# Optimization experiments

Measured on AMD Instinct MI355X. Metric: run time of the kernel, lower is better.

Reference implementation:

```python
import jax, jax.numpy as jnp
import numpy as np

D_MODEL = 1024
NUM_HEADS = 16
DK = D_MODEL // NUM_HEADS


def setup_inputs() -> dict:
    key = jax.random.key(0)
    ks = jax.random.split(key, 12)
    B, S, D = 2, 2048, D_MODEL
    s = 1.0 / np.sqrt(D)
    inp = {
        "Q": jax.random.normal(ks[0], (B, S, D), jnp.float32),
        "K": jax.random.normal(ks[1], (B, S, D), jnp.float32),
        "V": jax.random.normal(ks[2], (B, S, D), jnp.float32),
        "Wq": jax.random.uniform(ks[3], (D, D), jnp.float32, -s, s),
        "bq": jax.random.uniform(ks[4], (D,), jnp.float32, -s, s),
        "Wk": jax.random.uniform(ks[5], (D, D), jnp.float32, -s, s),
        "bk": jax.random.uniform(ks[6], (D,), jnp.float32, -s, s),
        "Wv": jax.random.uniform(ks[7], (D, D), jnp.float32, -s, s),
        "bv": jax.random.uniform(ks[8], (D,), jnp.float32, -s, s),
        "Wo": jax.random.uniform(ks[9], (D, D), jnp.float32, -s, s),
        "bo": jax.random.uniform(ks[10], (D,), jnp.float32, -s, s),
    }
    return inp


def reference(Q, K, V, Wq, bq, Wk, bk, Wv, bv, Wo, bo):
    B, S, D = Q.shape
    H, dk = NUM_HEADS, DK
    # projections (torch Linear: x @ W.T + b), split heads -> [B,H,S,dk]
    q = (Q @ Wq.T + bq).reshape(B, S, H, dk).transpose(0, 2, 1, 3)
    k = (K @ Wk.T + bk).reshape(B, S, H, dk).transpose(0, 2, 1, 3)
    v = (V @ Wv.T + bv).reshape(B, S, H, dk).transpose(0, 2, 1, 3)
    scores = jnp.einsum("bhqd,bhkd->bhqk", q, k) / jnp.sqrt(jnp.asarray(dk, q.dtype))
    attn = jax.nn.softmax(scores, axis=-1)
    out = jnp.einsum("bhqk,bhkd->bhqd", attn, v)  # [B,H,S,dk]
    out = out.transpose(0, 2, 1, 3).reshape(B, S, D)
    return out @ Wo.T + bo
```

## Files before the change

### kernel.cpp

```cpp
#include <hip/hip_runtime.h>
#include <stdint.h>


#define AS1 __attribute__((address_space(1)))
#define AS3 __attribute__((address_space(3)))

typedef unsigned short u16;
typedef short s16x8 __attribute__((ext_vector_type(8)));
typedef float f32x4 __attribute__((ext_vector_type(4)));
typedef float f32x16 __attribute__((ext_vector_type(16)));
typedef u16   u16x4 __attribute__((ext_vector_type(4)));

#if defined(__has_builtin)
#if __has_builtin(__builtin_amdgcn_exp2f)
#define EXP2F(x) __builtin_amdgcn_exp2f(x)
#else
#define EXP2F(x) exp2f(x)
#endif
#else
#define EXP2F(x) exp2f(x)
#endif

__device__ __forceinline__ u16 f2b(float f) {
  union { float f; uint32_t u; } v;
  v.f = f;
  uint32_t r = (v.u + 0x7fffu + ((v.u >> 16) & 1u)) >> 16;
  return (u16)r;
}

__device__ __forceinline__ uint32_t cvtpk(float lo, float hi) {
  uint32_t r;
  asm("v_cvt_pk_bf16_f32 %0, %1, %2" : "=v"(r) : "v"(lo), "v"(hi));
  return r;
}

__device__ __forceinline__ float max3f(float a, float b, float c) {
  float r;
  asm("v_max3_f32 %0, %1, %2, %3" : "=v"(r) : "v"(a), "v"(b), "v"(c));
  return r;
}

__device__ __forceinline__ f32x4 mfma16(s16x8 a, s16x8 b, f32x4 c) {
  return __builtin_amdgcn_mfma_f32_16x16x32_bf16(a, b, c, 0, 0, 0);
}

__device__ __forceinline__ f32x16 mfma32(s16x8 a, s16x8 b, f32x16 c) {
  return __builtin_amdgcn_mfma_f32_32x32x16_bf16(a, b, c, 0, 0, 0);
}

__device__ __forceinline__ s16x8 ld_g16(const u16* p) {
  return *reinterpret_cast<const s16x8*>(p);
}

__device__ __forceinline__ void stage16(const u16* g, u16* lds_base) {
  __builtin_amdgcn_global_load_lds((const AS1 unsigned int*)g,
                                   (AS3 unsigned int*)lds_base, 16, 0, 0);
}

struct CvtArgs {
  const float* src[4];
  u16* dst[4];
  int cum[5];
};

__global__ __launch_bounds__(256) void cvt_all(CvtArgs a) {
  const int bx = blockIdx.x;
  int seg = 0;
#pragma unroll
  for (int i = 1; i < 4; ++i) seg += (bx >= a.cum[i]) ? 1 : 0;
  const int off = (bx - a.cum[seg]) * 256 + threadIdx.x;
  float4 f = reinterpret_cast<const float4*>(a.src[seg])[off];
  union { u16 u[4]; uint64_t q; } o;
  o.u[0] = f2b(f.x); o.u[1] = f2b(f.y); o.u[2] = f2b(f.z); o.u[3] = f2b(f.w);
  reinterpret_cast<uint64_t*>(a.dst[seg])[off] = o.q;
}

template <int MODE>
__global__ __launch_bounds__(256) void gemm_bt(const float* __restrict__ Aq,
                                               const float* __restrict__ Ak,
                                               const float* __restrict__ Av,
                                               const u16* __restrict__ Abf,
                                               const u16* __restrict__ Wbase,
                                               const float* __restrict__ bias0,
                                               const float* __restrict__ bias1,
                                               const float* __restrict__ bias2,
                                               u16* __restrict__ outb,
                                               u16* __restrict__ vtout,
                                               float* __restrict__ outf) {
  __shared__ u16 As[2][128 * 64];
  __shared__ u16 Bs[2][128 * 64];
  const int tid = threadIdx.x;
  const int lane = tid & 63;
  const int w = tid >> 6;
  const int wr = w >> 1, wc = w & 1;

  const int bid = blockIdx.y * 8 + blockIdx.x;
  const int sw = (bid & 7) * 32 + (bid >> 3);
  const int n0 = (sw & 7) * 128;
  const int m0 = (sw >> 3) * 128;
  const int z = (MODE == 0) ? blockIdx.z : 0;
  const float QSC = 0.18033688011112042f;

  const float* Af = (MODE == 0) ? (z == 0 ? Aq : (z == 1 ? Ak : Av)) : nullptr;
  const u16* W = Wbase + (size_t)z * (1024u * 1024u);
  const float* bias = (MODE == 0) ? (z == 0 ? bias0 : (z == 1 ? bias1 : bias2)) : bias0;
  u16* ob = (MODE == 0) ? (outb + (size_t)z * (4096u * 1024u)) : nullptr;

  const int l15 = lane & 15, l4 = lane >> 4;

  const int sr = lane >> 3;
  const int sx = lane & 7;
  const float* gAf[4];
  const u16* gAb[4];
  const u16* gB[4];
#pragma unroll
  for (int j = 0; j < 4; ++j) {
    const int row = w * 32 + j * 8 + sr;
    const int lc = ((sx ^ (row & 7)) << 3);
    if (MODE == 0) gAf[j] = Af + (size_t)(m0 + row) * 1024 + lc;
    else           gAb[j] = Abf + (size_t)(m0 + row) * 1024 + lc;
    gB[j] = W + (size_t)(n0 + row) * 1024 + lc;
  }

  f32x4 acc[4][4];
#pragma unroll
  for (int i = 0; i < 4; ++i)
#pragma unroll
    for (int j = 0; j < 4; ++j) acc[i][j] = {0.f, 0.f, 0.f, 0.f};

#pragma unroll
  for (int j = 0; j < 4; ++j) {
    if (MODE == 0) {
      float4 b0 = *(const float4*)gAf[j];
      float4 b1 = *(const float4*)(gAf[j] + 4);
      union { uint32_t d[4]; s16x8 v; } cv;
      cv.d[0] = cvtpk(b0.x, b0.y); cv.d[1] = cvtpk(b0.z, b0.w);
      cv.d[2] = cvtpk(b1.x, b1.y); cv.d[3] = cvtpk(b1.z, b1.w);
      *(s16x8*)&As[0][(w * 32 + j * 8) * 64 + lane * 8] = cv.v;
    } else {
      stage16(gAb[j], &As[0][(w * 32 + j * 8) * 64]);
    }
    stage16(gB[j], &Bs[0][(w * 32 + j * 8) * 64]);
  }
  __syncthreads();

#pragma unroll 2
  for (int t = 0; t < 16; ++t) {
    const int cur = t & 1;
    float4 a0[4], a1[4];
    const bool more = (t + 1 < 16);
    if (more) {
      const int kt = (t + 1) * 64;
      if (MODE == 0) {
#pragma unroll
        for (int j = 0; j < 4; ++j) {
          a0[j] = *(const float4*)(gAf[j] + kt);
          a1[j] = *(const float4*)(gAf[j] + kt + 4);
        }
      } else {
#pragma unroll
        for (int j = 0; j < 4; ++j)
          stage16(gAb[j] + kt, &As[cur ^ 1][(w * 32 + j * 8) * 64]);
      }
#pragma unroll
      for (int j = 0; j < 4; ++j)
        stage16(gB[j] + kt, &Bs[cur ^ 1][(w * 32 + j * 8) * 64]);
    }
#pragma unroll
    for (int ks = 0; ks < 2; ++ks) {
      s16x8 af[4], bf[4];
#pragma unroll
      for (int mi = 0; mi < 4; ++mi) {
        const int row = wr * 64 + mi * 16 + l15;
        const int sc_ = (((ks << 2) | l4) ^ (l15 & 7)) << 3;
        af[mi] = *(const s16x8*)&As[cur][row * 64 + sc_];
      }
#pragma unroll
      for (int ni = 0; ni < 4; ++ni) {
        const int row = wc * 64 + ni * 16 + l15;
        const int sc_ = (((ks << 2) | l4) ^ (l15 & 7)) << 3;
        bf[ni] = *(const s16x8*)&Bs[cur][row * 64 + sc_];
      }
      __builtin_amdgcn_s_setprio(1);
#pragma unroll
      for (int mi = 0; mi < 4; ++mi)
#pragma unroll
        for (int ni = 0; ni < 4; ++ni)
          acc[mi][ni] = mfma16(af[mi], bf[ni], acc[mi][ni]);
      __builtin_amdgcn_s_setprio(0);
    }
    if (more && MODE == 0) {
#pragma unroll
      for (int j = 0; j < 4; ++j) {
        union { uint32_t d[4]; s16x8 v; } cv;
        cv.d[0] = cvtpk(a0[j].x, a0[j].y); cv.d[1] = cvtpk(a0[j].z, a0[j].w);
        cv.d[2] = cvtpk(a1[j].x, a1[j].y); cv.d[3] = cvtpk(a1[j].z, a1[j].w);
        *(s16x8*)&As[cur ^ 1][(w * 32 + j * 8) * 64 + lane * 8] = cv.v;
      }
    }
    __syncthreads();
  }

#pragma unroll
  for (int ni = 0; ni < 4; ++ni) {
    const int col = n0 + wc * 64 + ni * 16 + l15;
    const float bv = bias[col];
#pragma unroll
    for (int mi = 0; mi < 4; ++mi) {
      const int row0 = m0 + wr * 64 + mi * 16 + l4 * 4;
      if (MODE == 0 && z == 2) {
        const int b = row0 >> 11, s0 = row0 & 2047;
        const int pos0 = (s0 & ~15) | ((s0 & 4) << 1) | ((s0 & 8) >> 1);
        const int h = col >> 6, d = col & 63;
        u16x4 pk = {f2b(acc[mi][ni][0] + bv), f2b(acc[mi][ni][1] + bv),
                    f2b(acc[mi][ni][2] + bv), f2b(acc[mi][ni][3] + bv)};
        *(u16x4*)&vtout[((size_t)(b * 16 + h) * 64 + d) * 2048 + pos0] = pk;
      } else {
#pragma unroll
        for (int r = 0; r < 4; ++r) {
          float val = acc[mi][ni][r] + bv;
          const int row = row0 + r;
          if (MODE == 0) {
            if (z == 0) val *= QSC;
            const int b = row >> 11, s = row & 2047;
            const int h = col >> 6, d = col & 63;
            ob[((size_t)(b * 16 + h) * 2048 + s) * 64 + d] = f2b(val);
          } else {
            outf[(size_t)row * 1024 + col] = val;
          }
        }
      }
    }
  }
}

__global__ __launch_bounds__(512, 2) void fattn(const u16* __restrict__ qp,
                                                const u16* __restrict__ kp,
                                                const u16* __restrict__ vt,
                                                u16* __restrict__ ao) {
  __shared__ u16 Kt[2][4096];
  __shared__ u16 Vt[2][4096];

  const int lane = threadIdx.x & 63;
  const int w = threadIdx.x >> 6;
  const int bh = blockIdx.y;
  const int b = bh >> 4, h = bh & 15;
  const int q0 = blockIdx.x * 256 + w * 32;
  const u16* qb = qp + (size_t)bh * (2048 * 64);
  const u16* kb = kp + (size_t)bh * (2048 * 64);
  const u16* vb = vt + (size_t)bh * (64 * 2048);
  const int l31 = lane & 31, hl = lane >> 5;
  const int x7 = l31 & 7;
  const float THR = 8.0f;

  const int srow = (w << 3) + (lane >> 3);
  const int c0 = (((lane & 7) ^ (srow & 7)) << 3);

  s16x8 qa[4];
#pragma unroll
  for (int kc = 0; kc < 4; ++kc)
    qa[kc] = ld_g16(qb + (size_t)(q0 + l31) * 64 + kc * 16 + hl * 8);

  f32x16 o[2];
  float lsum = 0.f;
  float mrun = 0.f;
#pragma unroll
  for (int r = 0; r < 16; ++r) { o[0][r] = 0.f; o[1][r] = 0.f; }

  stage16(kb + (size_t)srow * 64 + c0, &Kt[0][w * 512]);
  stage16(vb + (size_t)srow * 2048 + c0, &Vt[0][w * 512]);
  __syncthreads();

#pragma unroll 2
  for (int t = 0; t < 32; ++t) {
    const int cur = t & 1;
    if (t + 1 < 32) {
      const int kk = (t + 1) << 6;
      stage16(kb + (size_t)(kk + srow) * 64 + c0, &Kt[cur ^ 1][w * 512]);
      stage16(vb + (size_t)srow * 2048 + kk + c0, &Vt[cur ^ 1][w * 512]);
    }

    f32x16 sc[2];
#pragma unroll
    for (int r = 0; r < 16; ++r) { sc[0][r] = -mrun; sc[1][r] = -mrun; }
#pragma unroll
    for (int nk = 0; nk < 2; ++nk) {
      s16x8 kf[4];
#pragma unroll
      for (int kc = 0; kc < 4; ++kc)
        kf[kc] = *(const s16x8*)&Kt[cur][(nk * 32 + l31) * 64 +
                                         ((((kc << 1) | hl) ^ x7) << 3)];
      __builtin_amdgcn_s_setprio(1);
#pragma unroll
      for (int kc = 0; kc < 4; ++kc)
        sc[nk] = mfma32(kf[kc], qa[kc], sc[nk]);
      __builtin_amdgcn_s_setprio(0);
    }

    float m = -1e30f;
#pragma unroll
    for (int nk = 0; nk < 2; ++nk)
#pragma unroll
      for (int r = 0; r < 16; r += 2)
        m = max3f(m, sc[nk][r], sc[nk][r + 1]);
    m = fmaxf(m, __shfl_xor(m, 32));

    if (__any(m > THR)) {
      const float d = fmaxf(m, 0.f);
      mrun += d;
      const float alpha = EXP2F(-d);
      lsum *= alpha;
#pragma unroll
      for (int r = 0; r < 16; ++r) { sc[0][r] -= d; sc[1][r] -= d; }
#pragma unroll
      for (int r = 0; r < 16; ++r) {
        float ar = __shfl(alpha, (r & 3) + 8 * (r >> 2) + 4 * hl);
        o[0][r] *= ar; o[1][r] *= ar;
      }
    }

#pragma unroll
    for (int nk = 0; nk < 2; ++nk) {
      float p[16];
#pragma unroll
      for (int r = 0; r < 16; ++r) p[r] = EXP2F(sc[nk][r]);
#pragma unroll
      for (int r = 0; r < 16; ++r) lsum += p[r];
#pragma unroll
      for (int kc = 0; kc < 2; ++kc) {
        union { uint32_t d[4]; s16x8 v; } pa;
        pa.d[0] = cvtpk(p[kc * 8 + 0], p[kc * 8 + 1]);
        pa.d[1] = cvtpk(p[kc * 8 + 2], p[kc * 8 + 3]);
        pa.d[2] = cvtpk(p[kc * 8 + 4], p[kc * 8 + 5]);
        pa.d[3] = cvtpk(p[kc * 8 + 6], p[kc * 8 + 7]);
        const int chunk = nk * 4 + kc * 2 + hl;
#pragma unroll
        for (int dt = 0; dt < 2; ++dt) {
          s16x8 vf = *(const s16x8*)&Vt[cur][(dt * 32 + l31) * 64 +
                                             ((chunk ^ x7) << 3)];
          __builtin_amdgcn_s_setprio(1);
          o[dt] = mfma32(pa.v, vf, o[dt]);
          __builtin_amdgcn_s_setprio(0);
        }
      }
    }

    __syncthreads();
  }

  lsum += __shfl_xor(lsum, 32);
#pragma unroll
  for (int r = 0; r < 16; ++r) {
    const int qreg = (r & 3) + 8 * (r >> 2) + 4 * hl;
    const float inv = 1.0f / __shfl(lsum, qreg);
    const int row = b * 2048 + q0 + qreg;
#pragma unroll
    for (int dt = 0; dt < 2; ++dt)
      ao[(size_t)row * 1024 + h * 64 + dt * 32 + l31] = f2b(o[dt][r] * inv);
  }
}

extern "C" void kernel_launch(void* const* d_in, const int* in_sizes, int n_in,
                              void* d_out, int out_size, void* d_ws, size_t ws_size,
                              hipStream_t stream) {
  const float* Q  = (const float*)d_in[0];
  const float* K  = (const float*)d_in[1];
  const float* V  = (const float*)d_in[2];
  const float* Wq = (const float*)d_in[3];
  const float* bq = (const float*)d_in[4];
  const float* Wk = (const float*)d_in[5];
  const float* bk = (const float*)d_in[6];
  const float* Wv = (const float*)d_in[7];
  const float* bv = (const float*)d_in[8];
  const float* Wo = (const float*)d_in[9];
  const float* bo = (const float*)d_in[10];
  float* out = (float*)d_out;

  const size_t NI = (size_t)4096 * 1024;
  const size_t NW = (size_t)1024 * 1024;
  u16* WB  = (u16*)d_ws;
  u16* QKV = WB + 4 * NW;
  u16* VT  = QKV + 3 * NI;
  u16* AO  = VT + NI;

  CvtArgs ca;
  ca.src[0] = Wq; ca.dst[0] = WB;
  ca.src[1] = Wk; ca.dst[1] = WB + NW;
  ca.src[2] = Wv; ca.dst[2] = WB + 2 * NW;
  ca.src[3] = Wo; ca.dst[3] = WB + 3 * NW;
  ca.cum[0] = 0; ca.cum[1] = 1024; ca.cum[2] = 2048; ca.cum[3] = 3072; ca.cum[4] = 4096;
  cvt_all<<<dim3(4096), 256, 0, stream>>>(ca);

  gemm_bt<0><<<dim3(8, 32, 3), 256, 0, stream>>>(Q, K, V, nullptr, WB, bq, bk, bv,
                                                 QKV, VT, nullptr);
  fattn<<<dim3(8, 32), 512, 0, stream>>>(QKV, QKV + NI, VT, AO);
  gemm_bt<1><<<dim3(8, 32, 1), 256, 0, stream>>>(nullptr, nullptr, nullptr, AO,
                                                 WB + 3 * NW, bo, nullptr, nullptr,
                                                 nullptr, nullptr, out);
}
```

Measured before the change: 121.4 us.

## Triple-buffer LDS and use partial vmcnt barriers in projection GEMM and attention

The attention kernel moves from double- to triple-buffered K/V tiles, staging two tiles ahead. Each iteration now waits with a partial vmcnt on an explicit s_barrier instead of a full __syncthreads, so global loads stay in flight across the barrier. The fp32-input projection GEMM gets a hand-unrolled pipeline: a three-slot A buffer, global loads issued two tiles ahead into alternating register sets, and the bf16 convert/store overlapped with the MFMA work. This adds LDS use (which may cut occupancy for the 512-thread, two-blocks-per-CU attention kernel) and more registers, and it depends on the hand-set vmcnt counts being correct.

```diff
diff --git a/kernel.cpp b/kernel.cpp
--- a/kernel.cpp
+++ b/kernel.cpp
@@ -20,6 +20,14 @@
 #else
 #define EXP2F(x) exp2f(x)
 #endif
+
+#define BARC(N)                                                               \
+  do {                                                                        \
+    __builtin_amdgcn_sched_barrier(0);                                        \
+    asm volatile("s_waitcnt vmcnt(" #N ") lgkmcnt(0)" ::: "memory");          \
+    __builtin_amdgcn_s_barrier();                                             \
+    __builtin_amdgcn_sched_barrier(0);                                        \
+  } while (0)
 
 __device__ __forceinline__ u16 f2b(float f) {
   union { float f; uint32_t u; } v;
@@ -87,8 +95,8 @@
                                                u16* __restrict__ outb,
                                                u16* __restrict__ vtout,
                                                float* __restrict__ outf) {
-  __shared__ u16 As[2][128 * 64];
-  __shared__ u16 Bs[2][128 * 64];
+  __shared__ u16 As[3 * 8192];
+  __shared__ u16 Bs[2][8192];
   const int tid = threadIdx.x;
   const int lane = tid & 63;
   const int w = tid >> 6;
@@ -128,44 +136,11 @@
 #pragma unroll
     for (int j = 0; j < 4; ++j) acc[i][j] = {0.f, 0.f, 0.f, 0.f};
 
-#pragma unroll
-  for (int j = 0; j < 4; ++j) {
-    if (MODE == 0) {
-      float4 b0 = *(const float4*)gAf[j];
-      float4 b1 = *(const float4*)(gAf[j] + 4);
-      union { uint32_t d[4]; s16x8 v; } cv;
-      cv.d[0] = cvtpk(b0.x, b0.y); cv.d[1] = cvtpk(b0.z, b0.w);
-      cv.d[2] = cvtpk(b1.x, b1.y); cv.d[3] = cvtpk(b1.z, b1.w);
-      *(s16x8*)&As[0][(w * 32 + j * 8) * 64 + lane * 8] = cv.v;
-    } else {
-      stage16(gAb[j], &As[0][(w * 32 + j * 8) * 64]);
-    }
-    stage16(gB[j], &Bs[0][(w * 32 + j * 8) * 64]);
-  }
-  __syncthreads();
-
-#pragma unroll 2
-  for (int t = 0; t < 16; ++t) {
-    const int cur = t & 1;
-    float4 a0[4], a1[4];
-    const bool more = (t + 1 < 16);
-    if (more) {
-      const int kt = (t + 1) * 64;
-      if (MODE == 0) {
-#pragma unroll
-        for (int j = 0; j < 4; ++j) {
-          a0[j] = *(const float4*)(gAf[j] + kt);
-          a1[j] = *(const float4*)(gAf[j] + kt + 4);
-        }
-      } else {
-#pragma unroll
-        for (int j = 0; j < 4; ++j)
-          stage16(gAb[j] + kt, &As[cur ^ 1][(w * 32 + j * 8) * 64]);
-      }
-#pragma unroll
-      for (int j = 0; j < 4; ++j)
-        stage16(gB[j] + kt, &Bs[cur ^ 1][(w * 32 + j * 8) * 64]);
-    }
+  auto G_STAGEW = [&](int kt, u16* bbuf) {
+#pragma unroll
+    for (int j = 0; j < 4; ++j) stage16(gB[j] + kt, &bbuf[(w * 32 + j * 8) * 64]);
+  };
+  auto G_MFMA = [&](int aoff, const u16* bbuf) {
 #pragma unroll
     for (int ks = 0; ks < 2; ++ks) {
       s16x8 af[4], bf[4];
@@ -173,13 +148,13 @@
       for (int mi = 0; mi < 4; ++mi) {
         const int row = wr * 64 + mi * 16 + l15;
         const int sc_ = (((ks << 2) | l4) ^ (l15 & 7)) << 3;
-        af[mi] = *(const s16x8*)&As[cur][row * 64 + sc_];
+        af[mi] = *(const s16x8*)&As[aoff + row * 64 + sc_];
       }
 #pragma unroll
       for (int ni = 0; ni < 4; ++ni) {
         const int row = wc * 64 + ni * 16 + l15;
         const int sc_ = (((ks << 2) | l4) ^ (l15 & 7)) << 3;
-        bf[ni] = *(const s16x8*)&Bs[cur][row * 64 + sc_];
+        bf[ni] = *(const s16x8*)&bbuf[row * 64 + sc_];
       }
       __builtin_amdgcn_s_setprio(1);
 #pragma unroll
@@ -189,16 +164,88 @@
           acc[mi][ni] = mfma16(af[mi], bf[ni], acc[mi][ni]);
       __builtin_amdgcn_s_setprio(0);
     }
-    if (more && MODE == 0) {
+  };
+
+  if (MODE == 0) {
+    float4 se0[4], se1[4], so0[4], so1[4];
+    auto G_ISSUE_E = [&](int kt) {
+#pragma unroll
+      for (int j = 0; j < 4; ++j) { se0[j] = *(const float4*)(gAf[j] + kt);
+                                    se1[j] = *(const float4*)(gAf[j] + kt + 4); }
+    };
+    auto G_ISSUE_O = [&](int kt) {
+#pragma unroll
+      for (int j = 0; j < 4; ++j) { so0[j] = *(const float4*)(gAf[j] + kt);
+                                    so1[j] = *(const float4*)(gAf[j] + kt + 4); }
+    };
+    auto G_CVT_E = [&](int aoff) {
 #pragma unroll
       for (int j = 0; j < 4; ++j) {
         union { uint32_t d[4]; s16x8 v; } cv;
-        cv.d[0] = cvtpk(a0[j].x, a0[j].y); cv.d[1] = cvtpk(a0[j].z, a0[j].w);
-        cv.d[2] = cvtpk(a1[j].x, a1[j].y); cv.d[3] = cvtpk(a1[j].z, a1[j].w);
-        *(s16x8*)&As[cur ^ 1][(w * 32 + j * 8) * 64 + lane * 8] = cv.v;
-      }
+        cv.d[0] = cvtpk(se0[j].x, se0[j].y); cv.d[1] = cvtpk(se0[j].z, se0[j].w);
+        cv.d[2] = cvtpk(se1[j].x, se1[j].y); cv.d[3] = cvtpk(se1[j].z, se1[j].w);
+        *(s16x8*)&As[aoff + (w * 32 + j * 8) * 64 + lane * 8] = cv.v;
+      }
+    };
+    auto G_CVT_O = [&](int aoff) {
+#pragma unroll
+      for (int j = 0; j < 4; ++j) {
+        union { uint32_t d[4]; s16x8 v; } cv;
+        cv.d[0] = cvtpk(so0[j].x, so0[j].y); cv.d[1] = cvtpk(so0[j].z, so0[j].w);
+        cv.d[2] = cvtpk(so1[j].x, so1[j].y); cv.d[3] = cvtpk(so1[j].z, so1[j].w);
+        *(s16x8*)&As[aoff + (w * 32 + j * 8) * 64 + lane * 8] = cv.v;
+      }
+    };
+
+    G_STAGEW(0, Bs[0]);
+    G_ISSUE_E(0);
+    G_ISSUE_O(64);
+    G_CVT_E(0);
+    BARC(8);
+
+    int aoff_r = 0, aoff_w = 8192;
+    for (int it = 0; it < 7; ++it) {
+      const int t0 = 2 * it;
+      G_STAGEW((t0 + 1) * 64, Bs[1]);
+      G_ISSUE_E((t0 + 2) * 64);
+      G_CVT_O(aoff_w);
+      G_MFMA(aoff_r, Bs[0]);
+      BARC(8);
+      aoff_r = aoff_w; aoff_w = (aoff_w == 16384) ? 0 : aoff_w + 8192;
+      G_STAGEW((t0 + 2) * 64, Bs[0]);
+      G_ISSUE_O((t0 + 3) * 64);
+      G_CVT_E(aoff_w);
+      G_MFMA(aoff_r, Bs[1]);
+      BARC(8);
+      aoff_r = aoff_w; aoff_w = (aoff_w == 16384) ? 0 : aoff_w + 8192;
+    }
+    G_STAGEW(15 * 64, Bs[1]);
+    G_CVT_O(aoff_w);
+    G_MFMA(aoff_r, Bs[0]);
+    BARC(0);
+    aoff_r = aoff_w;
+    G_MFMA(aoff_r, Bs[1]);
+  } else {
+#pragma unroll
+    for (int j = 0; j < 4; ++j) {
+      stage16(gAb[j], &As[(w * 32 + j * 8) * 64]);
+      stage16(gB[j], &Bs[0][(w * 32 + j * 8) * 64]);
     }
     __syncthreads();
+#pragma unroll 2
+    for (int t = 0; t < 16; ++t) {
+      const int cur = t & 1;
+      if (t + 1 < 16) {
+        const int kt = (t + 1) * 64;
+#pragma unroll
+        for (int j = 0; j < 4; ++j) {
+          stage16(gAb[j] + kt, &As[(cur ^ 1) * 8192 + (w * 32 + j * 8) * 64]);
+          stage16(gB[j] + kt, &Bs[cur ^ 1][(w * 32 + j * 8) * 64]);
+        }
+      }
+      G_MFMA(cur * 8192, Bs[cur]);
+      __syncthreads();
+    }
   }
 
 #pragma unroll
@@ -238,8 +285,8 @@
                                                 const u16* __restrict__ kp,
                                                 const u16* __restrict__ vt,
                                                 u16* __restrict__ ao) {
-  __shared__ u16 Kt[2][4096];
-  __shared__ u16 Vt[2][4096];
+  __shared__ u16 Ksh[3 * 4096];
+  __shared__ u16 Vsh[3 * 4096];
 
   const int lane = threadIdx.x & 63;
   const int w = threadIdx.x >> 6;
@@ -267,19 +314,13 @@
 #pragma unroll
   for (int r = 0; r < 16; ++r) { o[0][r] = 0.f; o[1][r] = 0.f; }
 
-  stage16(kb + (size_t)srow * 64 + c0, &Kt[0][w * 512]);
-  stage16(vb + (size_t)srow * 2048 + c0, &Vt[0][w * 512]);
-  __syncthreads();
-
-#pragma unroll 2
-  for (int t = 0; t < 32; ++t) {
-    const int cur = t & 1;
-    if (t + 1 < 32) {
-      const int kk = (t + 1) << 6;
-      stage16(kb + (size_t)(kk + srow) * 64 + c0, &Kt[cur ^ 1][w * 512]);
-      stage16(vb + (size_t)srow * 2048 + kk + c0, &Vt[cur ^ 1][w * 512]);
-    }
-
+  auto F_STAGE = [&](int tt, int off) {
+    const int kk = tt << 6;
+    stage16(kb + (size_t)(kk + srow) * 64 + c0, &Ksh[off + w * 512]);
+    stage16(vb + (size_t)srow * 2048 + kk + c0, &Vsh[off + w * 512]);
+  };
+
+  auto F_COMPUTE = [&](int off) {
     f32x16 sc[2];
 #pragma unroll
     for (int r = 0; r < 16; ++r) { sc[0][r] = -mrun; sc[1][r] = -mrun; }
@@ -288,8 +329,8 @@
       s16x8 kf[4];
 #pragma unroll
       for (int kc = 0; kc < 4; ++kc)
-        kf[kc] = *(const s16x8*)&Kt[cur][(nk * 32 + l31) * 64 +
-                                         ((((kc << 1) | hl) ^ x7) << 3)];
+        kf[kc] = *(const s16x8*)&Ksh[off + (nk * 32 + l31) * 64 +
+                                     ((((kc << 1) | hl) ^ x7) << 3)];
       __builtin_amdgcn_s_setprio(1);
 #pragma unroll
       for (int kc = 0; kc < 4; ++kc)
@@ -336,17 +377,32 @@
         const int chunk = nk * 4 + kc * 2 + hl;
 #pragma unroll
         for (int dt = 0; dt < 2; ++dt) {
-          s16x8 vf = *(const s16x8*)&Vt[cur][(dt * 32 + l31) * 64 +
-                                             ((chunk ^ x7) << 3)];
+          s16x8 vf = *(const s16x8*)&Vsh[off + (dt * 32 + l31) * 64 +
+                                         ((chunk ^ x7) << 3)];
           __builtin_amdgcn_s_setprio(1);
           o[dt] = mfma32(pa.v, vf, o[dt]);
           __builtin_amdgcn_s_setprio(0);
         }
       }
     }
-
-    __syncthreads();
+  };
+
+  F_STAGE(0, 0);
+  F_STAGE(1, 4096);
+  BARC(2);
+
+  int f_r = 0, f_c = 4096, f_s = 8192;
+#pragma unroll 3
+  for (int t = 0; t < 30; ++t) {
+    F_STAGE(t + 2, f_s);
+    F_COMPUTE(f_r);
+    BARC(2);
+    const int tmp = f_r; f_r = f_c; f_c = f_s; f_s = tmp;
   }
+  F_COMPUTE(f_r);
+  BARC(0);
+  f_r = f_c;
+  F_COMPUTE(f_r);
 
   lsum += __shfl_xor(lsum, 32);
 #pragma unroll
```

Measured after the change: 124.4 us. 2.5% more time.
